# Performance work log

Hardware: AMD Instinct MI355X
Metric: run time of the kernel (lower is better)

The kernel has to match this reference:

```python
import jax, jax.numpy as jnp
import numpy as np

K, D = 512, 256
NUM_CLASSES, SHARED_KEYS = 10, 10
B, H, W = 32, 64, 64
TRAINING = True


def setup_inputs() -> dict:
    key = jax.random.key(0)
    k1, k2, k3 = jax.random.split(key, 3)
    z_e_x = jax.random.normal(k1, (B, D, H, W), dtype=jnp.float32)
    labels = jax.random.randint(k2, (B,), 0, NUM_CLASSES)
    # nn.Embedding weight initialized uniform(-1/K, 1/K)
    codebook = jax.random.uniform(k3, (K, D), minval=-1.0 / K, maxval=1.0 / K,
                                  dtype=jnp.float32)
    return {"z_e_x": z_e_x, "codebook": codebook, "labels": labels}


def _irrelevant_regions(labels_flat, k, num_classes, n_shared, training):
    # uniform partition of the first K - n_shared codes over the classes
    uniform = jnp.round(jnp.linspace(-0.5, num_classes - 0.51, k - n_shared))  # [K-Ns]
    irrel = uniform[None, :] != labels_flat[:, None].astype(uniform.dtype)     # [N, K-Ns]
    n = labels_flat.shape[0]
    if training:
        tail = jnp.ones((n, n_shared), dtype=bool)   # TRAIN: shared keys masked out
    else:
        tail = jnp.zeros((n, n_shared), dtype=bool)
    return jnp.concatenate([irrel, tail], axis=1)    # [N, K]


def reference(z_e_x, codebook, labels):
    x = jnp.transpose(z_e_x, (0, 2, 3, 1))           # [B,H,W,D]
    xf = x.reshape(-1, D)                            # [N,D], N=B*H*W
    labels_flat = jnp.repeat(labels, H * W)          # [N]

    irrel = _irrelevant_regions(labels_flat, K, NUM_CLASSES, SHARED_KEYS, TRAINING)

    cb_sqr = jnp.sum(codebook * codebook, axis=1)                      # [K]
    in_sqr = jnp.sum(xf * xf, axis=1, keepdims=True)                   # [N,1]
    distances = in_sqr + cb_sqr[None, :] - 2.0 * (xf @ codebook.T)     # [N,K]
    distances = jnp.where(irrel, jnp.inf, distances)

    idx = jnp.argmin(distances, axis=1)                                # [N]

    codes = codebook[idx].reshape(x.shape)                             # [B,H,W,D]
    # straight-through path (detached codebook in torch)
    z_q = x + jax.lax.stop_gradient(codes - x)
    z_q_x = jnp.transpose(z_q, (0, 3, 1, 2))                           # [B,D,H,W]
    # non-detached codebook lookup path
    z_q_bar = codebook[jax.lax.stop_gradient(idx)].reshape(x.shape)
    z_q_x_bar = jnp.transpose(z_q_bar, (0, 3, 1, 2))                   # [B,D,H,W]
    return (z_q_x, z_q_x_bar)
```

## Files before the change

kernel.cpp:

```cpp
#include <hip/hip_runtime.h>


#define D       256
#define KCODES  512
#define HW      4096
#define BATCH   32
#define NPTS    (BATCH * HW)
#define WPW     13

__constant__ int c_cls_start[11] = {0, 51, 101, 151, 201, 251, 301, 352, 402, 452, 502};

__global__ __launch_bounds__(256) void prep_kernel(const float* __restrict__ cb,
                                                   float* __restrict__ cbT,
                                                   float* __restrict__ cbs) {
    const int k = blockIdx.x;
    const int d = threadIdx.x;
    float v = cb[k * D + d];
    cbT[(size_t)d * KCODES + k] = v;
    __shared__ double red[256];
    red[d] = (double)v * (double)v;
    __syncthreads();
    for (int s = 128; s > 0; s >>= 1) {
        if (d < s) red[d] += red[d + s];
        __syncthreads();
    }
    if (d == 0) cbs[k] = (float)red[0];
}

__global__ __launch_bounds__(256) void vq_kernel(const float* __restrict__ z,
                                                 const int* __restrict__ labels,
                                                 const float* __restrict__ cbT,
                                                 const float* __restrict__ cbs,
                                                 float* __restrict__ out) {
    const int lane = threadIdx.x & 63;
    const int w    = __builtin_amdgcn_readfirstlane(threadIdx.x >> 6);
    const int b    = blockIdx.x >> 6;
    const int hw   = ((blockIdx.x & 63) << 6) | lane;
    const int lab  = __builtin_amdgcn_readfirstlane(labels[b]);
    const int c0   = c_cls_start[lab];
    const int cnt  = c_cls_start[lab + 1] - c0;
    const int kbase = c0 + w * WPW;
    const int myn   = min(WPW, cnt - w * WPW);

    const float* __restrict__ xp = z + (size_t)b * (D * HW) + hw;

    float acc[WPW];
#pragma unroll
    for (int j = 0; j < WPW; ++j) acc[j] = 0.0f;

    double xsq = 0.0;

    float xb[4];
#pragma unroll
    for (int i = 0; i < 4; ++i) xb[i] = xp[(size_t)i * HW];

    for (int d = 0; d < D; d += 4) {
        float xn[4];
#pragma unroll
        for (int i = 0; i < 4; ++i) {
            int dn = (d + 4 + i) & (D - 1);
            xn[i] = xp[(size_t)dn * HW];
        }
#pragma unroll
        for (int i = 0; i < 4; ++i) {
            const float* __restrict__ wd = cbT + (size_t)(d + i) * KCODES + kbase;
            const float x = xb[i];
            xsq = fma((double)x, (double)x, xsq);
#pragma unroll
            for (int j = 0; j < WPW; ++j)
                acc[j] = fmaf(x, wd[j], acc[j]);
        }
#pragma unroll
        for (int i = 0; i < 4; ++i) xb[i] = xn[i];
    }

    const float insq = (float)xsq;
    float best = __builtin_inff();
    int bi = kbase;
#pragma unroll
    for (int j = 0; j < WPW; ++j) {
        if (j < myn) {
            float T    = insq + cbs[kbase + j];
            float dist = fmaf(-2.0f, acc[j], T);
            if (dist < best) { best = dist; bi = kbase + j; }
        }
    }

    __shared__ float sd[4][64];
    __shared__ int   si[4][64];
    sd[w][lane] = best;
    si[w][lane] = bi;
    __syncthreads();
    float fb = sd[0][lane];
    int   fi = si[0][lane];
#pragma unroll
    for (int w2 = 1; w2 < 4; ++w2) {
        float dv = sd[w2][lane];
        if (dv < fb) { fb = dv; fi = si[w2][lane]; }
    }

    float* __restrict__ o0 = out + (size_t)b * (D * HW) + hw;
    float* __restrict__ o1 = o0 + (size_t)NPTS * D;
    const int d0 = w * 64;
    for (int d = d0; d < d0 + 64; ++d) {
        float v = cbT[(size_t)d * KCODES + fi];
        o0[(size_t)d * HW] = v;
        o1[(size_t)d * HW] = v;
    }
}

extern "C" void kernel_launch(void* const* d_in, const int* in_sizes, int n_in,
                              void* d_out, int out_size, void* d_ws, size_t ws_size,
                              hipStream_t stream) {
    const float* z      = (const float*)d_in[0];
    const float* cb     = (const float*)d_in[1];
    const int*   labels = (const int*)d_in[2];
    float* out = (float*)d_out;

    float* cbT = (float*)d_ws;
    float* cbs = cbT + (size_t)D * KCODES;

    hipLaunchKernelGGL(prep_kernel, dim3(KCODES), dim3(D), 0, stream, cb, cbT, cbs);
    hipLaunchKernelGGL(vq_kernel, dim3(NPTS / 64), dim3(256), 0, stream,
                       z, labels, cbT, cbs, out);
}
```

Before: 406.7 us.

## Process four points per thread with float4 loads and stores

Each thread now handles four consecutive spatial points instead of one. Every codebook value loaded is reused across four accumulators, and the input reads and output writes become 16-byte float4 accesses. The grid shrinks by a factor of four, and the final argmin reduction and the gather are restructured through shared memory. The per-thread accumulator count grows from 13 to 52 floats plus four double sums, which raises register pressure and may lower occupancy.

After: 422.7 us. 4.0% more time.

```diff
diff --git a/kernel.cpp b/kernel.cpp
--- a/kernel.cpp
+++ b/kernel.cpp
@@ -7,6 +7,7 @@
 #define BATCH   32
 #define NPTS    (BATCH * HW)
 #define WPW     13
+#define PTS     256
 
 __constant__ int c_cls_start[11] = {0, 51, 101, 151, 201, 251, 301, 352, 402, 452, 502};
 
@@ -34,78 +35,109 @@
                                                  float* __restrict__ out) {
     const int lane = threadIdx.x & 63;
     const int w    = __builtin_amdgcn_readfirstlane(threadIdx.x >> 6);
-    const int b    = blockIdx.x >> 6;
-    const int hw   = ((blockIdx.x & 63) << 6) | lane;
+    const int b    = blockIdx.x >> 4;
+    const int hw0  = (blockIdx.x & 15) << 8;
+    const int p4   = hw0 | (lane << 2);
     const int lab  = __builtin_amdgcn_readfirstlane(labels[b]);
     const int c0   = c_cls_start[lab];
     const int cnt  = c_cls_start[lab + 1] - c0;
     const int kbase = c0 + w * WPW;
     const int myn   = min(WPW, cnt - w * WPW);
 
-    const float* __restrict__ xp = z + (size_t)b * (D * HW) + hw;
+    const float* __restrict__ xp = z + (size_t)b * (D * HW) + p4;
 
-    float acc[WPW];
+    float acc[WPW][4];
 #pragma unroll
-    for (int j = 0; j < WPW; ++j) acc[j] = 0.0f;
+    for (int j = 0; j < WPW; ++j)
+#pragma unroll
+        for (int p = 0; p < 4; ++p) acc[j][p] = 0.0f;
 
-    double xsq = 0.0;
+    double xsq[4] = {0.0, 0.0, 0.0, 0.0};
 
-    float xb[4];
+    float4 xb[4];
 #pragma unroll
-    for (int i = 0; i < 4; ++i) xb[i] = xp[(size_t)i * HW];
+    for (int i = 0; i < 4; ++i) xb[i] = *(const float4*)(xp + (size_t)i * HW);
 
     for (int d = 0; d < D; d += 4) {
-        float xn[4];
+        float4 xn[4];
 #pragma unroll
         for (int i = 0; i < 4; ++i) {
             int dn = (d + 4 + i) & (D - 1);
-            xn[i] = xp[(size_t)dn * HW];
+            xn[i] = *(const float4*)(xp + (size_t)dn * HW);
         }
 #pragma unroll
         for (int i = 0; i < 4; ++i) {
             const float* __restrict__ wd = cbT + (size_t)(d + i) * KCODES + kbase;
-            const float x = xb[i];
-            xsq = fma((double)x, (double)x, xsq);
+            const float4 x = xb[i];
+            xsq[0] = fma((double)x.x, (double)x.x, xsq[0]);
+            xsq[1] = fma((double)x.y, (double)x.y, xsq[1]);
+            xsq[2] = fma((double)x.z, (double)x.z, xsq[2]);
+            xsq[3] = fma((double)x.w, (double)x.w, xsq[3]);
 #pragma unroll
-            for (int j = 0; j < WPW; ++j)
-                acc[j] = fmaf(x, wd[j], acc[j]);
+            for (int j = 0; j < WPW; ++j) {
+                const float c = wd[j];
+                acc[j][0] = fmaf(x.x, c, acc[j][0]);
+                acc[j][1] = fmaf(x.y, c, acc[j][1]);
+                acc[j][2] = fmaf(x.z, c, acc[j][2]);
+                acc[j][3] = fmaf(x.w, c, acc[j][3]);
+            }
         }
 #pragma unroll
         for (int i = 0; i < 4; ++i) xb[i] = xn[i];
     }
 
-    const float insq = (float)xsq;
-    float best = __builtin_inff();
-    int bi = kbase;
+    __shared__ float sd[4][PTS];
+    __shared__ int   si[4][PTS];
 #pragma unroll
-    for (int j = 0; j < WPW; ++j) {
-        if (j < myn) {
-            float T    = insq + cbs[kbase + j];
-            float dist = fmaf(-2.0f, acc[j], T);
-            if (dist < best) { best = dist; bi = kbase + j; }
+    for (int p = 0; p < 4; ++p) {
+        const float insq = (float)xsq[p];
+        float best = __builtin_inff();
+        int bi = kbase;
+#pragma unroll
+        for (int j = 0; j < WPW; ++j) {
+            if (j < myn) {
+                float T    = insq + cbs[kbase + j];
+                float dist = fmaf(-2.0f, acc[j][p], T);
+                if (dist < best) { best = dist; bi = kbase + j; }
+            }
         }
+        sd[w][(lane << 2) + p] = best;
+        si[w][(lane << 2) + p] = bi;
     }
+    __syncthreads();
 
-    __shared__ float sd[4][64];
-    __shared__ int   si[4][64];
-    sd[w][lane] = best;
-    si[w][lane] = bi;
+    __shared__ int fidx[PTS];
+    {
+        const int pi = threadIdx.x;
+        float fb = sd[0][pi];
+        int   fi = si[0][pi];
+#pragma unroll
+        for (int w2 = 1; w2 < 4; ++w2) {
+            float dv = sd[w2][pi];
+            if (dv < fb) { fb = dv; fi = si[w2][pi]; }
+        }
+        fidx[pi] = fi;
+    }
     __syncthreads();
-    float fb = sd[0][lane];
-    int   fi = si[0][lane];
-#pragma unroll
-    for (int w2 = 1; w2 < 4; ++w2) {
-        float dv = sd[w2][lane];
-        if (dv < fb) { fb = dv; fi = si[w2][lane]; }
-    }
 
-    float* __restrict__ o0 = out + (size_t)b * (D * HW) + hw;
+    int f0 = fidx[(lane << 2) + 0];
+    int f1 = fidx[(lane << 2) + 1];
+    int f2 = fidx[(lane << 2) + 2];
+    int f3 = fidx[(lane << 2) + 3];
+
+    float* __restrict__ o0 = out + (size_t)b * (D * HW) + p4;
     float* __restrict__ o1 = o0 + (size_t)NPTS * D;
     const int d0 = w * 64;
+    const float* __restrict__ cbd = cbT + (size_t)d0 * KCODES;
     for (int d = d0; d < d0 + 64; ++d) {
-        float v = cbT[(size_t)d * KCODES + fi];
-        o0[(size_t)d * HW] = v;
-        o1[(size_t)d * HW] = v;
+        float4 v;
+        v.x = cbd[f0];
+        v.y = cbd[f1];
+        v.z = cbd[f2];
+        v.w = cbd[f3];
+        *(float4*)(o0 + (size_t)d * HW) = v;
+        *(float4*)(o1 + (size_t)d * HW) = v;
+        cbd += KCODES;
     }
 }
 
@@ -121,6 +153,6 @@
     float* cbs = cbT + (size_t)D * KCODES;
 
     hipLaunchKernelGGL(prep_kernel, dim3(KCODES), dim3(D), 0, stream, cb, cbT, cbs);
-    hipLaunchKernelGGL(vq_kernel, dim3(NPTS / 64), dim3(256), 0, stream,
+    hipLaunchKernelGGL(vq_kernel, dim3(NPTS / PTS), dim3(256), 0, stream,
                        z, labels, cbT, cbs, out);
 }
```
